# Kernel optimization log

Measured on AMD Instinct MI355X. Metric: run time of the kernel, lower is better.

Reference implementation:

```python
import jax, jax.numpy as jnp
import numpy as np

ALPHA = 0.001          # choice_alpha
GAMMA = 0.01           # count_penalty_gamma
NUM_CLASSES = 10


def setup_inputs() -> dict:
    key = jax.random.key(0)
    k1, k2, k3 = jax.random.split(key, 3)
    B, D, M = 1024, 784, 256
    x = jax.random.uniform(k1, (B, D), dtype=jnp.float32)
    templates = jax.random.uniform(k2, (M, 2 * D), dtype=jnp.float32)
    committed = jnp.ones((M,), dtype=bool)
    # arange % 10 guarantees every class has at least one category
    category_labels = jnp.arange(M, dtype=jnp.int32) % NUM_CLASSES
    category_counts = jax.random.randint(k3, (M,), 0, 1000).astype(jnp.int32)
    return {
        "x": x,
        "templates": templates,
        "committed": committed,
        "category_labels": category_labels,
        "category_counts": category_counts,
    }


def reference(x, templates, committed, category_labels, category_counts):
    # global min-max normalization (as in forward)
    x = (x - x.min()) / (x.max() - x.min() + 1e-10)
    # complement coding: [B, 2D]
    coded = jnp.concatenate([x, 1.0 - x], axis=-1)
    # fuzzy AND against every template: [B, M, 2D] (dominant intermediate)
    fuzzy = jnp.minimum(coded[:, None, :], templates[None, :, :])
    numerator = fuzzy.sum(axis=-1)                                   # [B, M]
    denominator = ALPHA + templates.sum(axis=-1) + GAMMA * category_counts.astype(jnp.float32)  # [M]
    choice = numerator / denominator[None, :]                         # [B, M]
    choice = jnp.where(committed[None, :], choice, -jnp.inf)
    # per-class logits: max choice over categories carrying each label
    logits = jax.ops.segment_max(choice.T, category_labels, num_segments=NUM_CLASSES).T  # [B, 10]
    return logits
```

## Files before the change

kernel.cpp:

```cpp
#include <hip/hip_runtime.h>
#include <math.h>

#define ALPHA 0.001f
#define GAMMA 0.01f
#define DD 784
#define TD 1568
#define RB 2048
#define MM 256
#define BB 1024
#define NCLS 10
#define ROWS_PB 4
#define TPW 4
#define NBLK 4096


#define TMPL_OFF 16384
#define CODED_OFF 540672

static __device__ __forceinline__ unsigned sad_u8(unsigned a, unsigned b, unsigned c) {
  unsigned d;
  asm("v_sad_u8 %0, %1, %2, %3" : "=v"(d) : "v"(a), "v"(b), "v"(c));
  return d;
}

template <int CTRL, int RMASK>
static __device__ __forceinline__ int dpp_iadd(int v) {
  int t = __builtin_amdgcn_update_dpp(0, v, CTRL, RMASK, 0xf, false);
  return v + t;
}
static __device__ __forceinline__ int wave_isum64_lane63(int v) {
  v = dpp_iadd<0x111, 0xf>(v);
  v = dpp_iadd<0x112, 0xf>(v);
  v = dpp_iadd<0x114, 0xf>(v);
  v = dpp_iadd<0x118, 0xf>(v);
  v = dpp_iadd<0x142, 0xa>(v);
  v = dpp_iadd<0x143, 0xc>(v);
  return v;
}

static __device__ __forceinline__ unsigned q8(float v) {
  return (unsigned)(v * 255.f + 0.5f);
}

__global__ __launch_bounds__(256) void k_minmax(const float* __restrict__ x,
                                                float* __restrict__ ws,
                                                int* __restrict__ out_bits) {
  const float4* x4 = (const float4*)x;
  const int n4 = BB * DD / 4;
  int tid = blockIdx.x * 256 + threadIdx.x;
  if (tid < BB * NCLS) out_bits[tid] = (int)0xFF800000;
  float mn = 1e30f, mx = -1e30f;
  for (int i = tid; i < n4; i += 256 * 256) {
    float4 v = x4[i];
    mn = fminf(mn, fminf(fminf(v.x, v.y), fminf(v.z, v.w)));
    mx = fmaxf(mx, fmaxf(fmaxf(v.x, v.y), fmaxf(v.z, v.w)));
  }
#pragma unroll
  for (int off = 32; off; off >>= 1) {
    mn = fminf(mn, __shfl_xor(mn, off, 64));
    mx = fmaxf(mx, __shfl_xor(mx, off, 64));
  }
  __shared__ float smn[4], smx[4];
  int lane = threadIdx.x & 63, wid = threadIdx.x >> 6;
  if (lane == 0) { smn[wid] = mn; smx[wid] = mx; }
  __syncthreads();
  if (threadIdx.x == 0) {
    mn = fminf(fminf(smn[0], smn[1]), fminf(smn[2], smn[3]));
    mx = fmaxf(fmaxf(smx[0], smx[1]), fmaxf(smx[2], smx[3]));
    ws[blockIdx.x] = mn;
    ws[256 + blockIdx.x] = mx;
  }
}

__global__ __launch_bounds__(64) void k_denom(const float* __restrict__ T,
                                              const int* __restrict__ committed,
                                              const int* __restrict__ counts,
                                              float* __restrict__ ws) {
  int m = blockIdx.x;
  int lane = threadIdx.x;

  if (m == 0) {
    float mn = 1e30f, mx = -1e30f;
    for (int i = lane; i < 256; i += 64) {
      mn = fminf(mn, ws[i]);
      mx = fmaxf(mx, ws[256 + i]);
    }
#pragma unroll
    for (int off = 32; off; off >>= 1) {
      mn = fminf(mn, __shfl_xor(mn, off, 64));
      mx = fmaxf(mx, __shfl_xor(mx, off, 64));
    }
    if (lane == 0) {
      ws[768] = mn;
      ws[769] = 1.0f / (mx - mn + 1e-10f);
    }
  }

  float s = 0.f;
  int isum = 0;
  uint4 pk[2] = {make_uint4(0,0,0,0), make_uint4(0,0,0,0)};
  if (lane < 49) {
    const float4* tp = (const float4*)(T + (size_t)m * TD + lane * 32);
    unsigned w[8];
#pragma unroll
    for (int d = 0; d < 8; ++d) {
      float4 f = tp[d];
      s += (f.x + f.y) + (f.z + f.w);
      unsigned b0 = q8(f.x), b1 = q8(f.y), b2 = q8(f.z), b3 = q8(f.w);
      isum += (int)(b0 + b1 + b2 + b3);
      w[d] = b0 | (b1 << 8) | (b2 << 16) | (b3 << 24);
    }
    pk[0] = make_uint4(w[0], w[1], w[2], w[3]);
    pk[1] = make_uint4(w[4], w[5], w[6], w[7]);
  }
  uint4* u8T = (uint4*)((char*)ws + TMPL_OFF + (size_t)m * RB);
  u8T[lane * 2]     = pk[0];
  u8T[lane * 2 + 1] = pk[1];
#pragma unroll
  for (int off = 32; off; off >>= 1) {
    s += __shfl_xor(s, off, 64);
    isum += __shfl_xor(isum, off, 64);
  }
  if (lane == 0) {
    float denom = ALPHA + s + GAMMA * (float)counts[m];
    ws[512 + m] = committed[m] ? (1.0f / denom) : -1.0f;
    ((int*)ws)[1024 + m] = isum;
  }
}

__global__ __launch_bounds__(256) void k_code(const float* __restrict__ x,
                                              float* __restrict__ ws) {
  __shared__ int rsum[4];
  int tid = threadIdx.x;
  if (tid < 4) rsum[tid] = 0;
  __syncthreads();
  float fmn = ws[768], finv = ws[769];
  float na = finv, nb = -fmn * finv;
  int row0 = blockIdx.x * 4;
  uint4* out4 = (uint4*)((char*)ws + CODED_OFF) + (size_t)blockIdx.x * 512;
#pragma unroll
  for (int i = 0; i < 2; ++i) {
    int idx = i * 256 + tid;
    int r = idx >> 7;
    int u = idx & 127;
    uint4 o = make_uint4(0, 0, 0, 0);
    if (u < 98) {
      int half = (u >= 49);
      int e = (half ? (u - 49) : u) * 16;
      const float4* xr = (const float4*)(x + (size_t)(row0 + r) * DD + e);
      unsigned w[4];
      int isum = 0;
#pragma unroll
      for (int d = 0; d < 4; ++d) {
        float4 f = xr[d];
        float v0 = na * f.x + nb, v1 = na * f.y + nb;
        float v2 = na * f.z + nb, v3 = na * f.w + nb;
        if (half) { v0 = 1.f - v0; v1 = 1.f - v1; v2 = 1.f - v2; v3 = 1.f - v3; }
        unsigned b0 = q8(v0), b1 = q8(v1), b2 = q8(v2), b3 = q8(v3);
        isum += (int)(b0 + b1 + b2 + b3);
        w[d] = b0 | (b1 << 8) | (b2 << 16) | (b3 << 24);
      }
      o = make_uint4(w[0], w[1], w[2], w[3]);
      atomicAdd(&rsum[r], isum);
    }
    out4[idx] = o;
  }
  __syncthreads();
  if (tid < 4) ((int*)ws)[1536 + row0 + tid] = rsum[tid];
}

__global__ __launch_bounds__(256) void k_main(const int* __restrict__ labels,
                                              const float* __restrict__ ws,
                                              int* __restrict__ out_bits) {
  __shared__ int clsmax[ROWS_PB][NCLS];

  int tid = threadIdx.x;
  int lane = tid & 63, wid = tid >> 6;
  int rg = blockIdx.x & 255;
  int tg = blockIdx.x >> 8;
  int row0 = rg * ROWS_PB;
  int m0 = tg * 16 + wid * TPW;

  const uint4* tbase = (const uint4*)((const char*)ws + TMPL_OFF);
  const uint4* cg = (const uint4*)((const char*)ws + CODED_OFF) + (size_t)row0 * 128;
  uint4 tr[TPW][2], cr[ROWS_PB][2];
#pragma unroll
  for (int t = 0; t < TPW; ++t) {
    const uint4* a0 = tbase + (size_t)(m0 + t) * 128 + lane;
    const uint4* a1 = a0 + 64;
    asm volatile("global_load_dwordx4 %0, %1, off" : "=v"(tr[t][0]) : "v"(a0));
    asm volatile("global_load_dwordx4 %0, %1, off" : "=v"(tr[t][1]) : "v"(a1));
  }
#pragma unroll
  for (int r = 0; r < ROWS_PB; ++r) {
    const uint4* b0 = cg + r * 128 + lane;
    const uint4* b1 = b0 + 64;
    asm volatile("global_load_dwordx4 %0, %1, off" : "=v"(cr[r][0]) : "v"(b0));
    asm volatile("global_load_dwordx4 %0, %1, off" : "=v"(cr[r][1]) : "v"(b1));
  }

  float scv[TPW];
  int lbv[TPW], tsv[TPW];
#pragma unroll
  for (int t = 0; t < TPW; ++t) {
    scv[t] = ws[512 + m0 + t];
    lbv[t] = labels[m0 + t];
    tsv[t] = ((const int*)ws)[1024 + m0 + t];
  }
  int myrow = ((const int*)ws)[1536 + row0 + (lane & 3)];

  if (tid < ROWS_PB * NCLS) clsmax[tid / NCLS][tid % NCLS] = (int)0xFF800000;

  asm volatile("s_waitcnt vmcnt(0)" ::: "memory");
  __builtin_amdgcn_sched_barrier(0);
  __syncthreads();

  unsigned acc[TPW][ROWS_PB];
#pragma unroll
  for (int t = 0; t < TPW; ++t)
#pragma unroll
    for (int r = 0; r < ROWS_PB; ++r) acc[t][r] = 0;

#pragma unroll
  for (int r = 0; r < ROWS_PB; ++r) {
#pragma unroll
    for (int t = 0; t < TPW; ++t) {
      unsigned a = acc[t][r];
      a = sad_u8(cr[r][0].x, tr[t][0].x, a);
      a = sad_u8(cr[r][0].y, tr[t][0].y, a);
      a = sad_u8(cr[r][0].z, tr[t][0].z, a);
      a = sad_u8(cr[r][0].w, tr[t][0].w, a);
      a = sad_u8(cr[r][1].x, tr[t][1].x, a);
      a = sad_u8(cr[r][1].y, tr[t][1].y, a);
      a = sad_u8(cr[r][1].z, tr[t][1].z, a);
      a = sad_u8(cr[r][1].w, tr[t][1].w, a);
      acc[t][r] = a;
    }
  }

  float sc = -1.f; int lb = 0, tsum_s = 0;
#pragma unroll
  for (int t = 0; t < TPW; ++t)
    if ((lane >> 2) == t) { sc = scv[t]; lb = lbv[t]; tsum_s = tsv[t]; }

  float vout = 0.f;
#pragma unroll
  for (int t = 0; t < TPW; ++t)
#pragma unroll
    for (int r = 0; r < ROWS_PB; ++r) {
      int s = wave_isum64_lane63((int)acc[t][r]);
      int g = __builtin_amdgcn_readlane(s, 63);
      if (lane == t * 4 + r)
        vout = (float)(myrow + tsum_s - g) * (sc * (0.5f / 255.f));
    }

  if (lane < 16 && sc > 0.f)
    atomicMax(&clsmax[lane & 3][lb], __float_as_int(vout));
  __syncthreads();

  if (tid < ROWS_PB * NCLS) {
    int rr = tid / NCLS, cc = tid - rr * NCLS;
    int bits = clsmax[rr][cc];
    if (bits != (int)0xFF800000)
      atomicMax(&out_bits[(row0 + rr) * NCLS + cc], bits);
  }
}

extern "C" void kernel_launch(void* const* d_in, const int* in_sizes, int n_in,
                              void* d_out, int out_size, void* d_ws, size_t ws_size,
                              hipStream_t stream) {
  const float* x = (const float*)d_in[0];
  const float* T = (const float*)d_in[1];
  const int* committed = (const int*)d_in[2];
  const int* labels = (const int*)d_in[3];
  const int* counts = (const int*)d_in[4];
  int* out_bits = (int*)d_out;
  float* ws = (float*)d_ws;

  k_minmax<<<dim3(256), dim3(256), 0, stream>>>(x, ws, out_bits);
  k_denom<<<dim3(256), dim3(64), 0, stream>>>(T, committed, counts, ws);
  k_code<<<dim3(256), dim3(256), 0, stream>>>(x, ws);
  k_main<<<dim3(NBLK), dim3(256), 0, stream>>>(labels, ws, out_bits);
}
```

Baseline: 29.74 us.

## Merge prep kernels, fold minmax finalisation, and double templates per wave

The final min/max reduction moves into k_minmax using a last-block-done atomic counter, which is reset each call by a memset. The template quantisation kernel and the input coding kernel are merged into one launch with block ranges split by role, cutting a kernel launch and its dependency gap. k_main now handles 8 templates per wave with half as many blocks, which amortises the coded-row loads over more templates but doubles the register footprint for template data. The added memset and the threadfence/atomic handshake add some serialisation of their own.

Result: slower. 36.55 us (+22.9%).

```diff
diff --git a/kernel.cpp b/kernel.cpp
--- a/kernel.cpp
+++ b/kernel.cpp
@@ -10,8 +10,8 @@
 #define BB 1024
 #define NCLS 10
 #define ROWS_PB 4
-#define TPW 4
-#define NBLK 4096
+#define TPW 8
+#define NBLK 2048
 
 
 #define TMPL_OFF 16384
@@ -47,10 +47,11 @@
                                                 int* __restrict__ out_bits) {
   const float4* x4 = (const float4*)x;
   const int n4 = BB * DD / 4;
-  int tid = blockIdx.x * 256 + threadIdx.x;
-  if (tid < BB * NCLS) out_bits[tid] = (int)0xFF800000;
+  int tid = threadIdx.x;
+  int gid = blockIdx.x * 256 + tid;
+  if (gid < BB * NCLS) out_bits[gid] = (int)0xFF800000;
   float mn = 1e30f, mx = -1e30f;
-  for (int i = tid; i < n4; i += 256 * 256) {
+  for (int i = gid; i < n4; i += 256 * 256) {
     float4 v = x4[i];
     mn = fminf(mn, fminf(fminf(v.x, v.y), fminf(v.z, v.w)));
     mx = fmaxf(mx, fmaxf(fmaxf(v.x, v.y), fmaxf(v.z, v.w)));
@@ -61,112 +62,117 @@
     mx = fmaxf(mx, __shfl_xor(mx, off, 64));
   }
   __shared__ float smn[4], smx[4];
-  int lane = threadIdx.x & 63, wid = threadIdx.x >> 6;
+  __shared__ bool amLast;
+  int lane = tid & 63, wid = tid >> 6;
   if (lane == 0) { smn[wid] = mn; smx[wid] = mx; }
   __syncthreads();
-  if (threadIdx.x == 0) {
+  if (tid == 0) {
     mn = fminf(fminf(smn[0], smn[1]), fminf(smn[2], smn[3]));
     mx = fmaxf(fmaxf(smx[0], smx[1]), fmaxf(smx[2], smx[3]));
     ws[blockIdx.x] = mn;
     ws[256 + blockIdx.x] = mx;
-  }
-}
-
-__global__ __launch_bounds__(64) void k_denom(const float* __restrict__ T,
+    __threadfence();
+    unsigned prev = atomicAdd((unsigned*)ws + 770, 1u);
+    amLast = (prev == 255);
+  }
+  __syncthreads();
+  if (amLast) {
+    __threadfence();
+    float m2 = ws[tid], x2 = ws[256 + tid];
+#pragma unroll
+    for (int off = 32; off; off >>= 1) {
+      m2 = fminf(m2, __shfl_xor(m2, off, 64));
+      x2 = fmaxf(x2, __shfl_xor(x2, off, 64));
+    }
+    if (lane == 0) { smn[wid] = m2; smx[wid] = x2; }
+    __syncthreads();
+    if (tid == 0) {
+      m2 = fminf(fminf(smn[0], smn[1]), fminf(smn[2], smn[3]));
+      x2 = fmaxf(fmaxf(smx[0], smx[1]), fmaxf(smx[2], smx[3]));
+      ws[768] = m2;
+      ws[769] = 1.0f / (x2 - m2 + 1e-10f);
+    }
+  }
+}
+
+__global__ __launch_bounds__(256) void k_prep(const float* __restrict__ x,
+                                              const float* __restrict__ T,
                                               const int* __restrict__ committed,
                                               const int* __restrict__ counts,
                                               float* __restrict__ ws) {
-  int m = blockIdx.x;
-  int lane = threadIdx.x;
-
-  if (m == 0) {
-    float mn = 1e30f, mx = -1e30f;
-    for (int i = lane; i < 256; i += 64) {
-      mn = fminf(mn, ws[i]);
-      mx = fmaxf(mx, ws[256 + i]);
-    }
-#pragma unroll
-    for (int off = 32; off; off >>= 1) {
-      mn = fminf(mn, __shfl_xor(mn, off, 64));
-      mx = fmaxf(mx, __shfl_xor(mx, off, 64));
-    }
-    if (lane == 0) {
-      ws[768] = mn;
-      ws[769] = 1.0f / (mx - mn + 1e-10f);
-    }
-  }
-
-  float s = 0.f;
-  int isum = 0;
-  uint4 pk[2] = {make_uint4(0,0,0,0), make_uint4(0,0,0,0)};
-  if (lane < 49) {
-    const float4* tp = (const float4*)(T + (size_t)m * TD + lane * 32);
-    unsigned w[8];
-#pragma unroll
-    for (int d = 0; d < 8; ++d) {
-      float4 f = tp[d];
-      s += (f.x + f.y) + (f.z + f.w);
-      unsigned b0 = q8(f.x), b1 = q8(f.y), b2 = q8(f.z), b3 = q8(f.w);
-      isum += (int)(b0 + b1 + b2 + b3);
-      w[d] = b0 | (b1 << 8) | (b2 << 16) | (b3 << 24);
-    }
-    pk[0] = make_uint4(w[0], w[1], w[2], w[3]);
-    pk[1] = make_uint4(w[4], w[5], w[6], w[7]);
-  }
-  uint4* u8T = (uint4*)((char*)ws + TMPL_OFF + (size_t)m * RB);
-  u8T[lane * 2]     = pk[0];
-  u8T[lane * 2 + 1] = pk[1];
-#pragma unroll
-  for (int off = 32; off; off >>= 1) {
-    s += __shfl_xor(s, off, 64);
-    isum += __shfl_xor(isum, off, 64);
-  }
-  if (lane == 0) {
-    float denom = ALPHA + s + GAMMA * (float)counts[m];
-    ws[512 + m] = committed[m] ? (1.0f / denom) : -1.0f;
-    ((int*)ws)[1024 + m] = isum;
-  }
-}
-
-__global__ __launch_bounds__(256) void k_code(const float* __restrict__ x,
-                                              float* __restrict__ ws) {
-  __shared__ int rsum[4];
   int tid = threadIdx.x;
-  if (tid < 4) rsum[tid] = 0;
-  __syncthreads();
-  float fmn = ws[768], finv = ws[769];
-  float na = finv, nb = -fmn * finv;
-  int row0 = blockIdx.x * 4;
-  uint4* out4 = (uint4*)((char*)ws + CODED_OFF) + (size_t)blockIdx.x * 512;
-#pragma unroll
-  for (int i = 0; i < 2; ++i) {
-    int idx = i * 256 + tid;
-    int r = idx >> 7;
-    int u = idx & 127;
-    uint4 o = make_uint4(0, 0, 0, 0);
-    if (u < 98) {
-      int half = (u >= 49);
-      int e = (half ? (u - 49) : u) * 16;
-      const float4* xr = (const float4*)(x + (size_t)(row0 + r) * DD + e);
-      unsigned w[4];
-      int isum = 0;
-#pragma unroll
-      for (int d = 0; d < 4; ++d) {
-        float4 f = xr[d];
-        float v0 = na * f.x + nb, v1 = na * f.y + nb;
-        float v2 = na * f.z + nb, v3 = na * f.w + nb;
-        if (half) { v0 = 1.f - v0; v1 = 1.f - v1; v2 = 1.f - v2; v3 = 1.f - v3; }
-        unsigned b0 = q8(v0), b1 = q8(v1), b2 = q8(v2), b3 = q8(v3);
+  int bid = blockIdx.x;
+  if (bid < 256) {
+    __shared__ int rsum[4];
+    if (tid < 4) rsum[tid] = 0;
+    __syncthreads();
+    float fmn = ws[768], finv = ws[769];
+    float na = finv, nb = -fmn * finv;
+    int row0 = bid * 4;
+    uint4* out4 = (uint4*)((char*)ws + CODED_OFF) + (size_t)bid * 512;
+#pragma unroll
+    for (int i = 0; i < 2; ++i) {
+      int idx = i * 256 + tid;
+      int r = idx >> 7;
+      int u = idx & 127;
+      uint4 o = make_uint4(0, 0, 0, 0);
+      if (u < 98) {
+        int half = (u >= 49);
+        int e = (half ? (u - 49) : u) * 16;
+        const float4* xr = (const float4*)(x + (size_t)(row0 + r) * DD + e);
+        unsigned w[4];
+        int isum = 0;
+#pragma unroll
+        for (int d = 0; d < 4; ++d) {
+          float4 f = xr[d];
+          float v0 = na * f.x + nb, v1 = na * f.y + nb;
+          float v2 = na * f.z + nb, v3 = na * f.w + nb;
+          if (half) { v0 = 1.f - v0; v1 = 1.f - v1; v2 = 1.f - v2; v3 = 1.f - v3; }
+          unsigned b0 = q8(v0), b1 = q8(v1), b2 = q8(v2), b3 = q8(v3);
+          isum += (int)(b0 + b1 + b2 + b3);
+          w[d] = b0 | (b1 << 8) | (b2 << 16) | (b3 << 24);
+        }
+        o = make_uint4(w[0], w[1], w[2], w[3]);
+        atomicAdd(&rsum[r], isum);
+      }
+      out4[idx] = o;
+    }
+    __syncthreads();
+    if (tid < 4) ((int*)ws)[1536 + row0 + tid] = rsum[tid];
+  } else {
+    int lane = tid & 63, wid = tid >> 6;
+    int m = (bid - 256) * 4 + wid;
+    float s = 0.f;
+    int isum = 0;
+    uint4 pk[2] = {make_uint4(0,0,0,0), make_uint4(0,0,0,0)};
+    if (lane < 49) {
+      const float4* tp = (const float4*)(T + (size_t)m * TD + lane * 32);
+      unsigned w[8];
+#pragma unroll
+      for (int d = 0; d < 8; ++d) {
+        float4 f = tp[d];
+        s += (f.x + f.y) + (f.z + f.w);
+        unsigned b0 = q8(f.x), b1 = q8(f.y), b2 = q8(f.z), b3 = q8(f.w);
         isum += (int)(b0 + b1 + b2 + b3);
         w[d] = b0 | (b1 << 8) | (b2 << 16) | (b3 << 24);
       }
-      o = make_uint4(w[0], w[1], w[2], w[3]);
-      atomicAdd(&rsum[r], isum);
-    }
-    out4[idx] = o;
-  }
-  __syncthreads();
-  if (tid < 4) ((int*)ws)[1536 + row0 + tid] = rsum[tid];
+      pk[0] = make_uint4(w[0], w[1], w[2], w[3]);
+      pk[1] = make_uint4(w[4], w[5], w[6], w[7]);
+    }
+    uint4* u8T = (uint4*)((char*)ws + TMPL_OFF + (size_t)m * RB);
+    u8T[lane * 2]     = pk[0];
+    u8T[lane * 2 + 1] = pk[1];
+#pragma unroll
+    for (int off = 32; off; off >>= 1) {
+      s += __shfl_xor(s, off, 64);
+      isum += __shfl_xor(isum, off, 64);
+    }
+    if (lane == 0) {
+      float denom = ALPHA + s + GAMMA * (float)counts[m];
+      ws[512 + m] = committed[m] ? (1.0f / denom) : -1.0f;
+      ((int*)ws)[1024 + m] = isum;
+    }
+  }
 }
 
 __global__ __launch_bounds__(256) void k_main(const int* __restrict__ labels,
@@ -179,7 +185,7 @@
   int rg = blockIdx.x & 255;
   int tg = blockIdx.x >> 8;
   int row0 = rg * ROWS_PB;
-  int m0 = tg * 16 + wid * TPW;
+  int m0 = tg * 32 + wid * TPW;
 
   const uint4* tbase = (const uint4*)((const char*)ws + TMPL_OFF);
   const uint4* cg = (const uint4*)((const char*)ws + CODED_OFF) + (size_t)row0 * 128;
@@ -254,7 +260,7 @@
         vout = (float)(myrow + tsum_s - g) * (sc * (0.5f / 255.f));
     }
 
-  if (lane < 16 && sc > 0.f)
+  if (lane < 32 && sc > 0.f)
     atomicMax(&clsmax[lane & 3][lb], __float_as_int(vout));
   __syncthreads();
 
@@ -277,8 +283,8 @@
   int* out_bits = (int*)d_out;
   float* ws = (float*)d_ws;
 
+  hipMemsetAsync((char*)d_ws + 770 * 4, 0, 4, stream);
   k_minmax<<<dim3(256), dim3(256), 0, stream>>>(x, ws, out_bits);
-  k_denom<<<dim3(256), dim3(64), 0, stream>>>(T, committed, counts, ws);
-  k_code<<<dim3(256), dim3(256), 0, stream>>>(x, ws);
+  k_prep<<<dim3(320), dim3(256), 0, stream>>>(x, T, committed, counts, ws);
   k_main<<<dim3(NBLK), dim3(256), 0, stream>>>(labels, ws, out_bits);
 }
```
